# Performance work log

Hardware: AMD Instinct MI355X
Metric: run time of the kernel (lower is better)

The kernel has to match this reference:

```python
import jax, jax.numpy as jnp
import numpy as np

T, D, H = 10, 45, 45  # time steps, input features, hidden size (hard-coded in source)


def _lstm_step(x, h, c, W_ih, W_hh, b_ih, b_hh):
    # PyTorch nn.LSTM single step; gate order i, f, g, o
    gates = x @ W_ih.T + b_ih + h @ W_hh.T + b_hh
    i, f, g, o = jnp.split(gates, 4, axis=-1)
    c2 = jax.nn.sigmoid(f) * c + jax.nn.sigmoid(i) * jnp.tanh(g)
    h2 = jax.nn.sigmoid(o) * jnp.tanh(c2)
    return h2, c2


def setup_inputs() -> dict:
    key = jax.random.key(0)
    ks = jax.random.split(key, 20)
    s = 0.1
    return {
        "price_input": jax.random.normal(ks[0], (T, D), dtype=jnp.float32),
        # encoder input attention: Linear(2H+T -> 1)
        "Wa": jax.random.normal(ks[1], (1, 2 * H + T), dtype=jnp.float32) * s,
        "ba": jax.random.normal(ks[2], (1,), dtype=jnp.float32) * s,
        # encoder LSTM
        "Wih_e": jax.random.normal(ks[3], (4 * H, D), dtype=jnp.float32) * s,
        "Whh_e": jax.random.normal(ks[4], (4 * H, H), dtype=jnp.float32) * s,
        "bih_e": jax.random.normal(ks[5], (4 * H,), dtype=jnp.float32) * s,
        "bhh_e": jax.random.normal(ks[6], (4 * H,), dtype=jnp.float32) * s,
        # decoder temporal attention: Linear(2H+D -> D), Tanh, Linear(D -> 1)
        "W1": jax.random.normal(ks[7], (D, 2 * H + D), dtype=jnp.float32) * s,
        "b1": jax.random.normal(ks[8], (D,), dtype=jnp.float32) * s,
        "W2": jax.random.normal(ks[9], (1, D), dtype=jnp.float32) * s,
        "b2": jax.random.normal(ks[10], (1,), dtype=jnp.float32) * s,
        # decoder LSTM (input dim = D)
        "Wih_d": jax.random.normal(ks[11], (4 * H, D), dtype=jnp.float32) * s,
        "Whh_d": jax.random.normal(ks[12], (4 * H, H), dtype=jnp.float32) * s,
        "bih_d": jax.random.normal(ks[13], (4 * H,), dtype=jnp.float32) * s,
        "bhh_d": jax.random.normal(ks[14], (4 * H,), dtype=jnp.float32) * s,
        # final fc: Linear(2H -> predict_size=45)
        "Wfc": jax.random.normal(ks[15], (45, 2 * H), dtype=jnp.float32) * s,
        "bfc": jax.random.normal(ks[16], (45,), dtype=jnp.float32) * s,
    }


def reference(price_input, Wa, ba, Wih_e, Whh_e, bih_e, bhh_e,
              W1, b1, W2, b2, Wih_d, Whh_d, bih_d, bhh_d, Wfc, bfc):
    x = price_input[None]                      # [1, T, D]
    xT = jnp.transpose(x, (0, 2, 1))           # [1, D, T]

    def enc_step(carry, x_t):
        h, c = carry                           # each [1, H]
        hr = jnp.broadcast_to(h[:, None, :], (1, D, H))
        cr = jnp.broadcast_to(c[:, None, :], (1, D, H))
        feat = jnp.concatenate([hr, cr, xT], axis=2)      # [1, D, 2H+T]
        scores = (feat @ Wa.T + ba)[..., 0]               # [1, D]
        attn = jax.nn.softmax(scores, axis=-1)            # over input features
        wi = attn * x_t[None]                             # [1, D]
        h2, c2 = _lstm_step(wi, h, c, Wih_e, Whh_e, bih_e, bhh_e)
        return (h2, c2), h2

    z = jnp.zeros((1, H), dtype=price_input.dtype)
    (_, _), hs = jax.lax.scan(enc_step, (z, z), price_input)
    price_vec = jnp.transpose(hs, (1, 0, 2))              # [1, T, H]

    # decoder: temporal attention over the T encoder states (hidden=cell=0)
    h0 = jnp.zeros((1, H), dtype=price_input.dtype)
    c0 = h0
    hr = jnp.broadcast_to(h0[:, None, :], (1, T, H))
    feat = jnp.concatenate([hr, hr, price_vec], axis=2)   # [1, T, 2H+D]
    scores = (jnp.tanh(feat @ W1.T + b1) @ W2.T + b2)[..., 0]  # [1, T]
    attn = jax.nn.softmax(scores, axis=-1)
    context = jnp.einsum('bt,bth->bh', attn, price_vec)   # [1, H]

    h1, _ = _lstm_step(context, h0, c0, Wih_d, Whh_d, bih_d, bhh_d)
    y_pred = jnp.concatenate([h1, context], axis=1) @ Wfc.T + bfc  # [1, 45]
    return y_pred
```

## Files before the change

kernel.cpp:

```cpp
#include <hip/hip_runtime.h>


static constexpr int NT = 10;
static constexpr int ND = 45;
static constexpr int NH = 45;
static constexpr int NG = 4 * NH;

__device__ __forceinline__ float rcp_(float x) { return __builtin_amdgcn_rcpf(x); }
__device__ __forceinline__ float sigf(float x) { return rcp_(1.0f + __expf(-x)); }
__device__ __forceinline__ float tanh_(float x) { return 1.0f - 2.0f * rcp_(1.0f + __expf(2.0f * x)); }

__global__ __launch_bounds__(256) void darnn_kernel(
    const float* __restrict__ X,
    const float* __restrict__ Wa,
    const float* __restrict__ Wih_e,
    const float* __restrict__ Whh_e,
    const float* __restrict__ bih_e,
    const float* __restrict__ bhh_e,
    const float* __restrict__ W1,
    const float* __restrict__ b1,
    const float* __restrict__ W2,
    const float* __restrict__ Wih_d,
    const float* __restrict__ bih_d,
    const float* __restrict__ bhh_d,
    const float* __restrict__ Wfc,
    const float* __restrict__ bfc,
    float* __restrict__ out)
{
    const int tid  = threadIdx.x;
    const int wave = tid >> 6;
    const int lane = tid & 63;
    const int g    = tid - 64;

    __shared__ float sR1[8100];
    __shared__ float sGx[NT * NG];
    __shared__ float sX[NT * ND];
    __shared__ float sWi[NT * ND];
    __shared__ float shs[NT * NH];
    __shared__ float sdec[NT * NH];
    __shared__ float sattn[ND];
    __shared__ float sat[NT];
    __shared__ float sctx[NH];
    __shared__ float sh1v[NH];
    __shared__ float sg[NG];
    __shared__ float sb1[ND];
    __shared__ float sW2v[ND];
    __shared__ float sbfcv[45];

    float wd[45];
    float bd = 0.0f, be = 0.0f;
    float4 re[11];

    {
        const float4* src = (const float4*)Whh_e;
        float4*       dst = (float4*)sR1;
#pragma unroll
        for (int k = 0; k < 8; ++k) {
            const int i = tid + k * 256;
            if (i < 2025) dst[i] = src[i];
        }
    }
    if (wave == 0) {
        const float2* x2 = (const float2*)X;
        float2*       d2 = (float2*)sX;
#pragma unroll
        for (int k = 0; k < 4; ++k) {
            const int i = lane + k * 64;
            if (i < 225) d2[i] = x2[i];
        }
    } else {
        if (g < NG) {
            const float* wrD = Wih_d + g * ND;
#pragma unroll
            for (int d = 0; d < 45; ++d) wd[d] = wrD[d];
            be = bih_e[g] + bhh_e[g];
            bd = bih_d[g] + bhh_d[g];
        }
        {
            const float4* src = (const float4*)Wih_e;
            const int s = tid - 64;
#pragma unroll
            for (int k = 0; k < 11; ++k) {
                const int i = s + k * 192;
                if (i < 2025) re[k] = src[i];
            }
        }
    }
    __syncthreads();

    float w0[45], w1[45], w2[45], w3[45];
    if (wave == 0) {
        const int j = (lane < 45) ? lane : 0;
#pragma unroll
        for (int k = 0; k < 45; ++k) {
            w0[k] = sR1[j * 45 + k];
            w1[k] = sR1[(45 + j) * 45 + k];
            w2[k] = sR1[(90 + j) * 45 + k];
            w3[k] = sR1[(135 + j) * 45 + k];
        }
    } else if (wave == 1) {
        float acc = -1e30f;
        if (lane < ND) {
            acc = 0.0f;
            for (int t = 0; t < NT; ++t) acc += Wa[90 + t] * sX[t * ND + lane];
        }
        float m = acc;
        for (int off = 32; off; off >>= 1) m = fmaxf(m, __shfl_xor(m, off, 64));
        float e = (lane < ND) ? __expf(acc - m) : 0.0f;
        float s = e;
        for (int off = 32; off; off >>= 1) s += __shfl_xor(s, off, 64);
        if (lane < ND) sattn[lane] = e * rcp_(s);
        __builtin_amdgcn_s_waitcnt(0);
        __builtin_amdgcn_wave_barrier();
        for (int i = lane; i < NT * ND; i += 64) sWi[i] = sattn[i % ND] * sX[i];
    }
    __syncthreads();

    if (wave > 0) {
        float4* dst = (float4*)sR1;
        const int s = tid - 64;
#pragma unroll
        for (int k = 0; k < 11; ++k) {
            const int i = s + k * 192;
            if (i < 2025) dst[i] = re[k];
        }
    }
    __syncthreads();

    if (wave > 0 && g < NG) {
        float we[45];
#pragma unroll
        for (int d = 0; d < 45; ++d) we[d] = sR1[g * 45 + d];
        float acc[NT];
#pragma unroll
        for (int t = 0; t < NT; ++t) acc[t] = be;
        for (int d = 0; d < ND; ++d) {
            const float wv = we[d];
#pragma unroll
            for (int t = 0; t < NT; ++t) acc[t] += wv * sWi[t * ND + d];
        }
#pragma unroll
        for (int t = 0; t < NT; ++t) sGx[t * NG + g] = acc[t];
    }
    __syncthreads();

    if (wave == 0) {
        const int j = (lane < 45) ? lane : 0;
        float h = 0.0f, c = 0.0f;
        for (int t = 0; t < NT; ++t) {
            float a0 = sGx[t * NG + j];
            float a1 = sGx[t * NG + 45 + j];
            float a2 = sGx[t * NG + 90 + j];
            float a3 = sGx[t * NG + 135 + j];
#pragma unroll
            for (int k = 0; k < 45; ++k) {
                const float hk = __shfl(h, k, 64);
                a0 += w0[k] * hk; a1 += w1[k] * hk;
                a2 += w2[k] * hk; a3 += w3[k] * hk;
            }
            c = sigf(a1) * c + sigf(a0) * tanh_(a2);
            h = sigf(a3) * tanh_(c);
            if (lane < 45) shs[t * NH + lane] = h;
        }
    } else {
        const int i0 = tid - 64;
        {
            const float2* s2 = (const float2*)Wfc;
            float2* d2 = (float2*)sR1;
            for (int i = i0; i < 2025; i += 192) d2[i] = s2[i];
        }
        for (int i = i0; i < ND * ND; i += 192) {
            const int r = i / 45, cc = i - r * 45;
            sR1[4050 + i] = W1[r * 135 + 90 + cc];
        }
        if (i0 < 45) { sb1[i0] = b1[i0]; sW2v[i0] = W2[i0]; sbfcv[i0] = bfc[i0]; }
    }
    __syncthreads();

    for (int i = tid; i < NT * NH; i += 256) {
        const int t = i / NH, k = i - t * NH;
        const float* wr = sR1 + 4050 + k * ND;
        const float* hv = shs + t * NH;
        float a = sb1[k];
        for (int jj = 0; jj < ND; ++jj) a += wr[jj] * hv[jj];
        sdec[i] = sW2v[k] * tanh_(a);
    }
    __syncthreads();

    if (tid < NT) {
        float a = 0.0f;
        for (int k = 0; k < NH; ++k) a += sdec[tid * NH + k];
        sat[tid] = a;
    }
    __syncthreads();
    if (tid == 0) {
        float m = -1e30f;
        for (int t = 0; t < NT; ++t) m = fmaxf(m, sat[t]);
        float e[NT], s = 0.0f;
        for (int t = 0; t < NT; ++t) { e[t] = __expf(sat[t] - m); s += e[t]; }
        const float inv = rcp_(s);
        for (int t = 0; t < NT; ++t) sat[t] = e[t] * inv;
    }
    __syncthreads();

    if (tid < NH) {
        float a = 0.0f;
        for (int t = 0; t < NT; ++t) a += sat[t] * shs[t * NH + tid];
        sctx[tid] = a;
    }
    __syncthreads();

    if (wave > 0 && g < NG) {
        float a = bd;
#pragma unroll
        for (int d = 0; d < 45; ++d) a += wd[d] * sctx[d];
        sg[g] = a;
    }
    __syncthreads();
    if (tid < NH) {
        const float ig = sigf(sg[tid]);
        const float gg = tanh_(sg[2 * NH + tid]);
        const float og = sigf(sg[3 * NH + tid]);
        sh1v[tid] = og * tanh_(ig * gg);
    }
    __syncthreads();

    if (tid < 45) {
        const float* wr = sR1 + tid * (2 * NH);
        float a = sbfcv[tid];
        for (int jj = 0; jj < NH; ++jj) a += wr[jj] * sh1v[jj];
        for (int jj = 0; jj < NH; ++jj) a += wr[NH + jj] * sctx[jj];
        out[tid] = a;
    }
}

extern "C" void kernel_launch(void* const* d_in, const int* in_sizes, int n_in,
                              void* d_out, int out_size, void* d_ws, size_t ws_size,
                              hipStream_t stream) {
    const float* X     = (const float*)d_in[0];
    const float* Wa    = (const float*)d_in[1];
    const float* Wih_e = (const float*)d_in[3];
    const float* Whh_e = (const float*)d_in[4];
    const float* bih_e = (const float*)d_in[5];
    const float* bhh_e = (const float*)d_in[6];
    const float* W1    = (const float*)d_in[7];
    const float* b1    = (const float*)d_in[8];
    const float* W2    = (const float*)d_in[9];
    const float* Wih_d = (const float*)d_in[11];
    const float* bih_d = (const float*)d_in[13];
    const float* bhh_d = (const float*)d_in[14];
    const float* Wfc   = (const float*)d_in[15];
    const float* bfc   = (const float*)d_in[16];
    float* out = (float*)d_out;

    darnn_kernel<<<dim3(1), dim3(256), 0, stream>>>(
        X, Wa, Wih_e, Whh_e, bih_e, bhh_e, W1, b1, W2,
        Wih_d, bih_d, bhh_d, Wfc, bfc, out);
}
```

Before: 108.9 us.

## Restructure prologue and cut block barriers with wave-local shuffles and raw barriers

New measurement: 106.8 us. 2.0% less time.

```diff
diff --git a/kernel.cpp b/kernel.cpp
--- a/kernel.cpp
+++ b/kernel.cpp
@@ -5,10 +5,20 @@
 static constexpr int ND = 45;
 static constexpr int NH = 45;
 static constexpr int NG = 4 * NH;
+static constexpr int SWS = 48;
 
 __device__ __forceinline__ float rcp_(float x) { return __builtin_amdgcn_rcpf(x); }
 __device__ __forceinline__ float sigf(float x) { return rcp_(1.0f + __expf(-x)); }
 __device__ __forceinline__ float tanh_(float x) { return 1.0f - 2.0f * rcp_(1.0f + __expf(2.0f * x)); }
+
+__device__ __forceinline__ void lds_flush() {
+    asm volatile("s_waitcnt lgkmcnt(0)" ::: "memory");
+}
+__device__ __forceinline__ void barrier_raw() {
+    __builtin_amdgcn_sched_barrier(0);
+    __builtin_amdgcn_s_barrier();
+    __builtin_amdgcn_sched_barrier(0);
+}
 
 __global__ __launch_bounds__(256) void darnn_kernel(
     const float* __restrict__ X,
@@ -32,61 +42,84 @@
     const int lane = tid & 63;
     const int g    = tid - 64;
 
-    __shared__ float sR1[8100];
+    __shared__ __align__(16) float sR1[8100];
+    __shared__ __align__(16) float sWi[NT * SWS];
     __shared__ float sGx[NT * NG];
-    __shared__ float sX[NT * ND];
-    __shared__ float sWi[NT * ND];
     __shared__ float shs[NT * NH];
     __shared__ float sdec[NT * NH];
-    __shared__ float sattn[ND];
     __shared__ float sat[NT];
     __shared__ float sctx[NH];
-    __shared__ float sh1v[NH];
     __shared__ float sg[NG];
     __shared__ float sb1[ND];
     __shared__ float sW2v[ND];
     __shared__ float sbfcv[45];
 
-    float wd[45];
-    float bd = 0.0f, be = 0.0f;
-    float4 re[11];
-
-    {
-        const float4* src = (const float4*)Whh_e;
-        float4*       dst = (float4*)sR1;
-#pragma unroll
-        for (int k = 0; k < 8; ++k) {
-            const int i = tid + k * 256;
-            if (i < 2025) dst[i] = src[i];
-        }
-    }
-    if (wave == 0) {
-        const float2* x2 = (const float2*)X;
-        float2*       d2 = (float2*)sX;
-#pragma unroll
-        for (int k = 0; k < 4; ++k) {
-            const int i = lane + k * 64;
-            if (i < 225) d2[i] = x2[i];
-        }
-    } else {
+    float we[45];
+    float be = 0.0f;
+
+    if (wave == 1) {
+        float xc[NT];
+        if (lane < ND) {
+#pragma unroll
+            for (int t = 0; t < NT; ++t) xc[t] = X[t * ND + lane];
+        }
+        float xi[8];
+#pragma unroll
+        for (int r = 0; r < 8; ++r) {
+            const int i = lane + r * 64;
+            xi[r] = (i < NT * ND) ? X[i] : 0.0f;
+        }
+        {
+            const float* wrE = Wih_e + g * ND;
+#pragma unroll
+            for (int d = 0; d < ND; ++d) we[d] = wrE[d];
+            be = bih_e[g] + bhh_e[g];
+        }
+        float acc = -1e30f;
+        if (lane < ND) {
+            acc = 0.0f;
+#pragma unroll
+            for (int t = 0; t < NT; ++t) acc += Wa[90 + t] * xc[t];
+        }
+        float m = acc;
+        for (int off = 32; off; off >>= 1) m = fmaxf(m, __shfl_xor(m, off, 64));
+        float e = (lane < ND) ? __expf(acc - m) : 0.0f;
+        float s = e;
+        for (int off = 32; off; off >>= 1) s += __shfl_xor(s, off, 64);
+        const float p = e * rcp_(s);
+#pragma unroll
+        for (int r = 0; r < 8; ++r) {
+            const int i  = lane + r * 64;
+            const int iw = (i < NT * ND) ? i : (NT * ND - 1);
+            const int t  = iw / ND, d = iw - t * ND;
+            const float av = __shfl(p, d, 64);
+            if (i < NT * ND) sWi[t * SWS + d] = av * xi[r];
+        }
+        lds_flush();
+    } else if (wave >= 2) {
+        const int b = tid - 128;
+        float4 wc[16];
+        const float4* s4 = (const float4*)Whh_e;
+#pragma unroll
+        for (int r = 0; r < 16; ++r) {
+            const int i = b + r * 128;
+            if (i < 2025) wc[r] = s4[i];
+        }
         if (g < NG) {
-            const float* wrD = Wih_d + g * ND;
-#pragma unroll
-            for (int d = 0; d < 45; ++d) wd[d] = wrD[d];
+            const float* wrE = Wih_e + g * ND;
+#pragma unroll
+            for (int d = 0; d < ND; ++d) we[d] = wrE[d];
             be = bih_e[g] + bhh_e[g];
-            bd = bih_d[g] + bhh_d[g];
-        }
-        {
-            const float4* src = (const float4*)Wih_e;
-            const int s = tid - 64;
-#pragma unroll
-            for (int k = 0; k < 11; ++k) {
-                const int i = s + k * 192;
-                if (i < 2025) re[k] = src[i];
-            }
-        }
-    }
-    __syncthreads();
+        }
+        float4* d4 = (float4*)sR1;
+#pragma unroll
+        for (int r = 0; r < 16; ++r) {
+            const int i = b + r * 128;
+            if (i < 2025) d4[i] = wc[r];
+        }
+        lds_flush();
+    }
+    barrier_raw();
 
     float w0[45], w1[45], w2[45], w3[45];
     if (wave == 0) {
@@ -98,52 +131,30 @@
             w2[k] = sR1[(90 + j) * 45 + k];
             w3[k] = sR1[(135 + j) * 45 + k];
         }
-    } else if (wave == 1) {
-        float acc = -1e30f;
-        if (lane < ND) {
-            acc = 0.0f;
-            for (int t = 0; t < NT; ++t) acc += Wa[90 + t] * sX[t * ND + lane];
-        }
-        float m = acc;
-        for (int off = 32; off; off >>= 1) m = fmaxf(m, __shfl_xor(m, off, 64));
-        float e = (lane < ND) ? __expf(acc - m) : 0.0f;
-        float s = e;
-        for (int off = 32; off; off >>= 1) s += __shfl_xor(s, off, 64);
-        if (lane < ND) sattn[lane] = e * rcp_(s);
-        __builtin_amdgcn_s_waitcnt(0);
-        __builtin_amdgcn_wave_barrier();
-        for (int i = lane; i < NT * ND; i += 64) sWi[i] = sattn[i % ND] * sX[i];
-    }
-    __syncthreads();
-
-    if (wave > 0) {
-        float4* dst = (float4*)sR1;
-        const int s = tid - 64;
-#pragma unroll
-        for (int k = 0; k < 11; ++k) {
-            const int i = s + k * 192;
-            if (i < 2025) dst[i] = re[k];
-        }
-    }
-    __syncthreads();
-
-    if (wave > 0 && g < NG) {
-        float we[45];
-#pragma unroll
-        for (int d = 0; d < 45; ++d) we[d] = sR1[g * 45 + d];
+    } else if (g < NG) {
         float acc[NT];
 #pragma unroll
         for (int t = 0; t < NT; ++t) acc[t] = be;
-        for (int d = 0; d < ND; ++d) {
-            const float wv = we[d];
-#pragma unroll
-            for (int t = 0; t < NT; ++t) acc[t] += wv * sWi[t * ND + d];
-        }
+#pragma unroll
+        for (int d4 = 0; d4 < 11; ++d4) {
+            const float wa = we[d4 * 4 + 0], wb = we[d4 * 4 + 1];
+            const float wc_ = we[d4 * 4 + 2], wd_ = we[d4 * 4 + 3];
+#pragma unroll
+            for (int t = 0; t < NT; ++t) {
+                const float4 v = *(const float4*)&sWi[t * SWS + d4 * 4];
+                acc[t] += wa * v.x + wb * v.y + wc_ * v.z + wd_ * v.w;
+            }
+        }
+#pragma unroll
+        for (int t = 0; t < NT; ++t) acc[t] += we[44] * sWi[t * SWS + 44];
 #pragma unroll
         for (int t = 0; t < NT; ++t) sGx[t * NG + g] = acc[t];
     }
-    __syncthreads();
-
+    lds_flush();
+    barrier_raw();
+
+    float wd[45];
+    float bd = 0.0f;
     if (wave == 0) {
         const int j = (lane < 45) ? lane : 0;
         float h = 0.0f, c = 0.0f;
@@ -174,8 +185,15 @@
             sR1[4050 + i] = W1[r * 135 + 90 + cc];
         }
         if (i0 < 45) { sb1[i0] = b1[i0]; sW2v[i0] = W2[i0]; sbfcv[i0] = bfc[i0]; }
-    }
-    __syncthreads();
+        if (g < NG) {
+            const float* wrD = Wih_d + g * ND;
+#pragma unroll
+            for (int d = 0; d < ND; ++d) wd[d] = wrD[d];
+            bd = bih_d[g] + bhh_d[g];
+        }
+    }
+    lds_flush();
+    barrier_raw();
 
     for (int i = tid; i < NT * NH; i += 256) {
         const int t = i / NH, k = i - t * NH;
@@ -185,30 +203,32 @@
         for (int jj = 0; jj < ND; ++jj) a += wr[jj] * hv[jj];
         sdec[i] = sW2v[k] * tanh_(a);
     }
-    __syncthreads();
-
-    if (tid < NT) {
-        float a = 0.0f;
-        for (int k = 0; k < NH; ++k) a += sdec[tid * NH + k];
-        sat[tid] = a;
-    }
-    __syncthreads();
-    if (tid == 0) {
-        float m = -1e30f;
-        for (int t = 0; t < NT; ++t) m = fmaxf(m, sat[t]);
-        float e[NT], s = 0.0f;
-        for (int t = 0; t < NT; ++t) { e[t] = __expf(sat[t] - m); s += e[t]; }
-        const float inv = rcp_(s);
-        for (int t = 0; t < NT; ++t) sat[t] = e[t] * inv;
-    }
-    __syncthreads();
+    lds_flush();
+    barrier_raw();
+
+    if (wave == 0) {
+        float a = -1e30f;
+        if (lane < NT) {
+            a = 0.0f;
+            for (int k = 0; k < NH; ++k) a += sdec[lane * NH + k];
+        }
+        float m = a;
+        for (int off = 8; off; off >>= 1) m = fmaxf(m, __shfl_xor(m, off, 16));
+        float e = (lane < NT) ? __expf(a - m) : 0.0f;
+        float s = e;
+        for (int off = 8; off; off >>= 1) s += __shfl_xor(s, off, 16);
+        if (lane < NT) sat[lane] = e * rcp_(s);
+    }
+    lds_flush();
+    barrier_raw();
 
     if (tid < NH) {
         float a = 0.0f;
         for (int t = 0; t < NT; ++t) a += sat[t] * shs[t * NH + tid];
         sctx[tid] = a;
     }
-    __syncthreads();
+    lds_flush();
+    barrier_raw();
 
     if (wave > 0 && g < NG) {
         float a = bd;
@@ -216,21 +236,26 @@
         for (int d = 0; d < 45; ++d) a += wd[d] * sctx[d];
         sg[g] = a;
     }
-    __syncthreads();
-    if (tid < NH) {
-        const float ig = sigf(sg[tid]);
-        const float gg = tanh_(sg[2 * NH + tid]);
-        const float og = sigf(sg[3 * NH + tid]);
-        sh1v[tid] = og * tanh_(ig * gg);
-    }
-    __syncthreads();
-
-    if (tid < 45) {
-        const float* wr = sR1 + tid * (2 * NH);
-        float a = sbfcv[tid];
-        for (int jj = 0; jj < NH; ++jj) a += wr[jj] * sh1v[jj];
-        for (int jj = 0; jj < NH; ++jj) a += wr[NH + jj] * sctx[jj];
-        out[tid] = a;
+    lds_flush();
+    barrier_raw();
+
+    if (wave == 0) {
+        float h1 = 0.0f, cxv = 0.0f;
+        if (lane < 45) {
+            const float ig = sigf(sg[lane]);
+            const float gg = tanh_(sg[2 * NH + lane]);
+            const float og = sigf(sg[3 * NH + lane]);
+            h1  = og * tanh_(ig * gg);
+            cxv = sctx[lane];
+        }
+        const float* wr = sR1 + ((lane < 45) ? lane : 0) * (2 * NH);
+        float a = (lane < 45) ? sbfcv[lane] : 0.0f;
+        for (int jj = 0; jj < NH; ++jj) {
+            const float h1j = __shfl(h1, jj, 64);
+            const float cxj = __shfl(cxv, jj, 64);
+            a += wr[jj] * h1j + wr[NH + jj] * cxj;
+        }
+        if (lane < 45) out[lane] = a;
     }
 }
 
```
